# Performance work log

Measured on AMD Instinct MI355X. Metric: run time of the kernel, lower is better.

Reference implementation:

```python
import jax, jax.numpy as jnp
import numpy as np

IN_DIM = 1024
OUT_DIM = 1024
L = 4
HIDDEN = 64
EMB_DIM = 2 + 2 * 2 * L  # 18
BATCH = 8192
W0 = 30.0


def make_embedded_coords():
    gy, gx = jnp.meshgrid(jnp.linspace(-1.0, 1.0, OUT_DIM), jnp.linspace(-1.0, 1.0, IN_DIM), indexing='ij')
    coords = jnp.stack([gy, gx], axis=-1).reshape(-1, 2)  # [rows*cols, 2]
    embeds = [coords]
    for i in range(L):
        freq = 2.0 ** i
        embeds.append(jnp.sin(freq * jnp.pi * coords))
        embeds.append(jnp.cos(freq * jnp.pi * coords))
    return jnp.concatenate(embeds, axis=-1)  # [rows*cols, 18]


def setup_inputs() -> dict:
    key = jax.random.key(0)
    ks = jax.random.split(key, 8)
    # init scales matching torch code
    u = lambda k, shape, b: jax.random.uniform(k, shape, jnp.float32, -b, b)
    W1 = u(ks[0], (HIDDEN, EMB_DIM), 1.0 / EMB_DIM)
    b1 = u(ks[1], (HIDDEN,), 1.0 / np.sqrt(EMB_DIM))
    s2 = np.sqrt(6.0 / HIDDEN) / W0
    W2 = u(ks[2], (HIDDEN, HIDDEN), s2)
    b2 = u(ks[3], (HIDDEN,), 1.0 / np.sqrt(HIDDEN))
    W3 = u(ks[4], (1, HIDDEN), s2)
    b3 = u(ks[5], (1,), 1.0 / np.sqrt(HIDDEN))
    x = jax.random.normal(ks[6], (BATCH, IN_DIM), jnp.float32)
    bias = jnp.zeros((OUT_DIM,), jnp.float32)
    return {
        'x': x,
        'embedded_coords': make_embedded_coords(),
        'W1': W1, 'b1': b1, 'W2': W2, 'b2': b2, 'W3': W3, 'b3': b3,
        'bias': bias,
    }


def reference(x, embedded_coords, W1, b1, W2, b2, W3, b3, bias):
    rows = bias.shape[0]
    cols = x.shape[-1]
    # tiny fully-fused hypernet MLP over rows*cols coordinate points
    h = jnp.sin(W0 * (embedded_coords @ W1.T + b1))  # [rows*cols, 64]
    h = jnp.sin(W0 * (h @ W2.T + b2))                # [rows*cols, 64]
    W = (h @ W3.T + b3).reshape(rows, cols)          # generated weight
    return x @ W.T + bias                            # [batch, out_dim]
```

## Files before the change

kernel.cpp:

```cpp
#include <hip/hip_runtime.h>
#include <hip/hip_bf16.h>


typedef __attribute__((ext_vector_type(8))) short bf16x8;
typedef __attribute__((ext_vector_type(4))) float f32x4;

#define SIN_SCALE 4.77464829275686f

__device__ __forceinline__ unsigned short f2bf(float f) {
    union { float f; unsigned u; } v; v.f = f;
    unsigned r = v.u + 0x7fffu + ((v.u >> 16) & 1u);
    return (unsigned short)(r >> 16);
}

__device__ __forceinline__ unsigned pktrunc(float a, float b) {
    union { float f; unsigned u; } x, y; x.f = a; y.f = b;
    return (x.u >> 16) | (y.u & 0xffff0000u);
}

__device__ __forceinline__ float sinrev(float x) {
    return __builtin_amdgcn_sinf(x);
}
__device__ __forceinline__ float cosrev(float x) {
    return __builtin_amdgcn_cosf(x);
}

__device__ __forceinline__ void async_ld16(const void* g, void* l) {
    __builtin_amdgcn_global_load_lds(
        (__attribute__((address_space(1))) void*)g,
        (__attribute__((address_space(3))) void*)l, 16, 0, 0);
}

__global__ __launch_bounds__(256) void tables_kernel(
        const float* __restrict__ ec,
        const float* __restrict__ W1, const float* __restrict__ b1,
        const float* __restrict__ W2, const float* __restrict__ b2,
        float2* __restrict__ SCrow, float2* __restrict__ SCcol,
        unsigned short* __restrict__ W2bf, float* __restrict__ b2s) {
    if (blockIdx.x == 512) {
        int tid = threadIdx.x;
        #pragma unroll
        for (int q = 0; q < 16; ++q) {
            int i = q * 256 + tid;
            unsigned u = __float_as_uint(SIN_SCALE * W2[i]);
            W2bf[i] = (unsigned short)(u >> 16);
        }
        if (tid < 64) b2s[tid] = SIN_SCALE * b2[tid];
        return;
    }
    int idx = blockIdx.x * 256 + threadIdx.x;
    int j = idx & 63;
    int t = idx >> 6;
    const float* wr = W1 + j * 18;
    if (t < 1024) {
        const float* pe = ec + (long)t * 1024 * 18;
        float z = b1[j];
        #pragma unroll
        for (int i = 0; i < 18; ++i) z += wr[i] * pe[i];
        z *= SIN_SCALE;
        SCrow[t * 64 + j] = make_float2(sinrev(z), cosrev(z));
    } else {
        int c = t - 1024;
        const float* pe = ec + (long)c * 18;
        float z = 0.f;
        #pragma unroll
        for (int i = 0; i < 18; ++i) z += wr[i] * (pe[i] - ec[i]);
        z *= SIN_SCALE;
        SCcol[c * 64 + j] = make_float2(sinrev(z), cosrev(z));
    }
}

__global__ __launch_bounds__(256) void fused_cast_siren(
        const float4* __restrict__ x, unsigned short* __restrict__ xb,
        const float2* __restrict__ SCrow, const float2* __restrict__ SCcol,
        const unsigned short* __restrict__ W2bf, const float* __restrict__ b2s,
        const float* __restrict__ W3, const float* __restrict__ b3,
        unsigned short* __restrict__ Wout) {
    __shared__ __align__(16) float2 zrow_l[16 * 64];
    __shared__ __align__(16) float2 zcol_l[32 * 64];

    int tid  = threadIdx.x;
    int sb   = blockIdx.x;
    int lane = tid & 63;
    int wv   = tid >> 6;
    int ln   = lane & 15;
    int kq   = lane >> 4;

    int br = sb & 63;
    int bc = sb >> 6;

    long ci = (long)sb * 1024 + tid;

    float4 cv0 = x[ci];
    float4 cv1 = x[ci + 256];

    {
        const float* rs = (const float*)SCrow + (long)br * 16 * 128;
        #pragma unroll
        for (int q = 0; q < 2; ++q) {
            int idx = q * 256 + tid;
            async_ld16(rs + idx * 4, (float*)zrow_l + (q * 256 + wv * 64) * 4);
        }
        #pragma unroll
        for (int q = 0; q < 4; ++q) {
            int P  = q * 256 + tid;
            int cr = P >> 5;
            int pc = P & 31;
            int lc = (pc & 16) | ((pc & 15) ^ (cr & 15));
            const float* src = (const float*)SCcol + (long)(bc * 32 + cr) * 128 + lc * 4;
            async_ld16(src, (float*)zcol_l + (q * 256 + wv * 64) * 4);
        }
    }

    {
        ushort4 o;
        o.x = f2bf(cv0.x); o.y = f2bf(cv0.y); o.z = f2bf(cv0.z); o.w = f2bf(cv0.w);
        *(ushort4*)(xb + ci * 4) = o;
        o.x = f2bf(cv1.x); o.y = f2bf(cv1.y); o.z = f2bf(cv1.z); o.w = f2bf(cv1.w);
        *(ushort4*)(xb + (ci + 256) * 4) = o;
    }
    float4 cv2 = x[ci + 512];
    float4 cv3 = x[ci + 768];

    bf16x8 wfrag[2][4];
    #pragma unroll
    for (int kc = 0; kc < 2; ++kc)
        #pragma unroll
        for (int nt = 0; nt < 4; ++nt)
            wfrag[kc][nt] = *(const bf16x8*)(W2bf + (nt * 16 + ln) * 64 + kc * 32 + kq * 8);
    f32x4 b2x4[4], w3x4[4];
    #pragma unroll
    for (int nt = 0; nt < 4; ++nt) {
        float4 bb = *(const float4*)(b2s + nt * 16 + kq * 4);
        float4 ww = *(const float4*)(W3 + nt * 16 + kq * 4);
        b2x4[nt][0] = bb.x; b2x4[nt][1] = bb.y; b2x4[nt][2] = bb.z; b2x4[nt][3] = bb.w;
        w3x4[nt][0] = ww.x; w3x4[nt][1] = ww.y; w3x4[nt][2] = ww.z; w3x4[nt][3] = ww.w;
    }
    float b3s = b3[0];

    {
        ushort4 o;
        o.x = f2bf(cv2.x); o.y = f2bf(cv2.y); o.z = f2bf(cv2.z); o.w = f2bf(cv2.w);
        *(ushort4*)(xb + (ci + 512) * 4) = o;
        o.x = f2bf(cv3.x); o.y = f2bf(cv3.y); o.z = f2bf(cv3.z); o.w = f2bf(cv3.w);
        *(ushort4*)(xb + (ci + 768) * 4) = o;
    }

    __syncthreads();

    #pragma unroll
    for (int lr4 = 0; lr4 < 4; ++lr4) {
        int lr = wv * 4 + lr4;
        const float2* zb = zrow_l + lr * 64 + kq * 8;
        float sr0[8], cr0[8], sr1[8], cr1[8];
        #pragma unroll
        for (int j = 0; j < 8; ++j) {
            float2 t0 = zb[j];      sr0[j] = t0.x; cr0[j] = t0.y;
            float2 t1 = zb[32 + j]; sr1[j] = t1.x; cr1[j] = t1.y;
        }

        #pragma unroll
        for (int ct = 0; ct < 2; ++ct) {
            int cl = ct * 16 + ln;
            const float2* cb2 = zcol_l + cl * 64;
            int sx = cl & 15;

            union { bf16x8 v; unsigned u[4]; } a0, a1;
            #pragma unroll
            for (int t = 0; t < 4; ++t) {
                int p0 = (((kq * 4 + t) ^ sx)) * 2;
                int p1 = ((16 | ((kq * 4 + t) ^ sx))) * 2;
                float h0[2], h1v[2];
                #pragma unroll
                for (int e = 0; e < 2; ++e) {
                    int j = t * 2 + e;
                    float2 c0 = cb2[p0 + e];
                    float2 c1 = cb2[p1 + e];
                    h0[e]  = fmaf(sr0[j], c0.y, cr0[j] * c0.x);
                    h1v[e] = fmaf(sr1[j], c1.y, cr1[j] * c1.x);
                }
                a0.u[t] = pktrunc(h0[0], h0[1]);
                a1.u[t] = pktrunc(h1v[0], h1v[1]);
            }

            f32x4 acc[4];
            #pragma unroll
            for (int nt = 0; nt < 4; ++nt) acc[nt] = b2x4[nt];
            #pragma unroll
            for (int nt = 0; nt < 4; ++nt) {
                acc[nt] = __builtin_amdgcn_mfma_f32_16x16x32_bf16(wfrag[0][nt], a0.v, acc[nt], 0, 0, 0);
                acc[nt] = __builtin_amdgcn_mfma_f32_16x16x32_bf16(wfrag[1][nt], a1.v, acc[nt], 0, 0, 0);
            }

            float ps[4] = {0.f, 0.f, 0.f, 0.f};
            #pragma unroll
            for (int nt = 0; nt < 4; ++nt)
                #pragma unroll
                for (int rg = 0; rg < 4; ++rg)
                    ps[rg] = fmaf(w3x4[nt][rg], sinrev(acc[nt][rg]), ps[rg]);
            float s = (ps[0] + ps[1]) + (ps[2] + ps[3]);
            s += __shfl_xor(s, 32, 64);
            s += __shfl_xor(s, 16, 64);

            if (kq == 0) {
                long o = (long)(br * 16 + lr) * 1024 + bc * 32 + ct * 16 + ln;
                Wout[o] = f2bf(s + b3s);
            }
        }
    }
}

__global__ __launch_bounds__(256) void gemm_kernel(
        const unsigned short* __restrict__ A,
        const unsigned short* __restrict__ B,
        const float* __restrict__ bias,
        float* __restrict__ C) {
    const int K = 1024;
    __shared__ __align__(16) unsigned short As[2][128 * 64];
    __shared__ __align__(16) unsigned short Bs[2][128 * 64];

    int tid  = threadIdx.x;
    int lane = tid & 63;
    int wv   = tid >> 6;
    int wm   = wv & 1, wn = wv >> 1;
    long Abase = (long)blockIdx.x * 128 * K;
    long Bbase = (long)blockIdx.y * 128 * K;

    int sr8 = tid >> 3;
    int sl  = tid & 7;
    int rsel = lane & 15;
    int kq   = lane >> 4;

    f32x4 acc[4][4] = {};

    auto stage = [&](int kt, int sbuf) {
        #pragma unroll
        for (int q = 0; q < 4; ++q) {
            int row = q * 32 + sr8;
            int cc  = sl ^ (row & 7);
            const unsigned short* ga = A + Abase + (long)row * K + kt + cc * 8;
            const unsigned short* gb = B + Bbase + (long)row * K + kt + cc * 8;
            unsigned short* la = &As[sbuf][(q * 256 + wv * 64) * 8];
            unsigned short* lb = &Bs[sbuf][(q * 256 + wv * 64) * 8];
            async_ld16(ga, la);
            async_ld16(gb, lb);
        }
    };

    auto compute = [&](int sbuf) {
        #pragma unroll
        for (int h = 0; h < 2; ++h) {
            bf16x8 af[4], bf[4];
            #pragma unroll
            for (int mi = 0; mi < 4; ++mi) {
                int row = wm * 64 + mi * 16 + rsel;
                int ch  = (h * 4 + kq) ^ (row & 7);
                af[mi] = *(const bf16x8*)&As[sbuf][row * 64 + ch * 8];
            }
            #pragma unroll
            for (int ni = 0; ni < 4; ++ni) {
                int row = wn * 64 + ni * 16 + rsel;
                int ch  = (h * 4 + kq) ^ (row & 7);
                bf[ni] = *(const bf16x8*)&Bs[sbuf][row * 64 + ch * 8];
            }
            #pragma unroll
            for (int mi = 0; mi < 4; ++mi)
                #pragma unroll
                for (int ni = 0; ni < 4; ++ni)
                    acc[mi][ni] = __builtin_amdgcn_mfma_f32_16x16x32_bf16(
                        af[mi], bf[ni], acc[mi][ni], 0, 0, 0);
        }
    };

    stage(0, 0);
    __syncthreads();
    int buf = 0;
    for (int kt = 64; kt < K; kt += 64) {
        stage(kt, buf ^ 1);
        compute(buf);
        __syncthreads();
        buf ^= 1;
    }
    compute(buf);

    int row0 = blockIdx.x * 128 + wm * 64;
    int col0 = blockIdx.y * 128 + wn * 64;
    #pragma unroll
    for (int ni = 0; ni < 4; ++ni) {
        int col = col0 + ni * 16 + rsel;
        float bv = bias[col];
        #pragma unroll
        for (int mi = 0; mi < 4; ++mi) {
            int rbase = row0 + mi * 16 + kq * 4;
            #pragma unroll
            for (int r = 0; r < 4; ++r)
                C[(long)(rbase + r) * 1024 + col] = acc[mi][ni][r] + bv;
        }
    }
}

extern "C" void kernel_launch(void* const* d_in, const int* in_sizes, int n_in,
                              void* d_out, int out_size, void* d_ws, size_t ws_size,
                              hipStream_t stream) {
    const float* x    = (const float*)d_in[0];
    const float* ec   = (const float*)d_in[1];
    const float* W1   = (const float*)d_in[2];
    const float* b1   = (const float*)d_in[3];
    const float* W2   = (const float*)d_in[4];
    const float* b2   = (const float*)d_in[5];
    const float* W3   = (const float*)d_in[6];
    const float* b3   = (const float*)d_in[7];
    const float* bias = (const float*)d_in[8];
    float* out = (float*)d_out;

    unsigned short* xb = (unsigned short*)d_ws;
    unsigned short* Wb = xb + (size_t)8192 * 1024;
    float2* SCrow = (float2*)(Wb + (size_t)1024 * 1024);
    float2* SCcol = SCrow + 1024 * 64;
    unsigned short* W2bf = (unsigned short*)(SCcol + 1024 * 64);
    float* b2s = (float*)(W2bf + 4096);

    tables_kernel<<<513, 256, 0, stream>>>(ec, W1, b1, W2, b2, SCrow, SCcol, W2bf, b2s);
    fused_cast_siren<<<2048, 256, 0, stream>>>((const float4*)x, xb, SCrow, SCcol,
                                               W2bf, b2s, W3, b3, Wb);
    dim3 g(64, 8);
    gemm_kernel<<<g, 256, 0, stream>>>(xb, Wb, bias, out);
}
```

Baseline: 183.6 us.

## Process four tiles per block with double-buffered LDS and pipelined loads

Each block of the fused cast/SIREN kernel now handles four consecutive tiles instead of one, and the grid shrinks from 2048 to 512 blocks. LDS tables are double-buffered, so the async loads of the next tile's row/column sin-cos tables and the next chunk of x overlap with the MFMA compute of the current tile. The bf16 cast stores for x are interleaved into the same software pipeline. This spreads the per-block setup (W2 fragments, biases) over more work. It doubles LDS per block and cuts the number of resident waves, which may reduce latency hiding for the memory-bound x cast.

```diff
diff --git a/kernel.cpp b/kernel.cpp
--- a/kernel.cpp
+++ b/kernel.cpp
@@ -76,30 +76,25 @@
         const unsigned short* __restrict__ W2bf, const float* __restrict__ b2s,
         const float* __restrict__ W3, const float* __restrict__ b3,
         unsigned short* __restrict__ Wout) {
-    __shared__ __align__(16) float2 zrow_l[16 * 64];
-    __shared__ __align__(16) float2 zcol_l[32 * 64];
+    __shared__ __align__(16) float2 zrow_l[2][16 * 64];
+    __shared__ __align__(16) float2 zcol_l[2][32 * 64];
 
     int tid  = threadIdx.x;
-    int sb   = blockIdx.x;
     int lane = tid & 63;
     int wv   = tid >> 6;
     int ln   = lane & 15;
     int kq   = lane >> 4;
 
-    int br = sb & 63;
-    int bc = sb >> 6;
-
-    long ci = (long)sb * 1024 + tid;
-
-    float4 cv0 = x[ci];
-    float4 cv1 = x[ci + 256];
-
-    {
+    int sb0 = blockIdx.x * 4;
+    long ci0 = (long)sb0 * 1024 + tid;
+
+    auto stage = [&](int st, int b) {
+        int br = st & 63, bc = st >> 6;
         const float* rs = (const float*)SCrow + (long)br * 16 * 128;
         #pragma unroll
         for (int q = 0; q < 2; ++q) {
             int idx = q * 256 + tid;
-            async_ld16(rs + idx * 4, (float*)zrow_l + (q * 256 + wv * 64) * 4);
+            async_ld16(rs + idx * 4, (float*)&zrow_l[b][0] + (q * 256 + wv * 64) * 4);
         }
         #pragma unroll
         for (int q = 0; q < 4; ++q) {
@@ -108,19 +103,29 @@
             int pc = P & 31;
             int lc = (pc & 16) | ((pc & 15) ^ (cr & 15));
             const float* src = (const float*)SCcol + (long)(bc * 32 + cr) * 128 + lc * 4;
-            async_ld16(src, (float*)zcol_l + (q * 256 + wv * 64) * 4);
-        }
-    }
-
-    {
+            async_ld16(src, (float*)&zcol_l[b][0] + (q * 256 + wv * 64) * 4);
+        }
+    };
+
+    auto cld = [&](long ci, float4& v0, float4& v1, float4& v2, float4& v3) {
+        v0 = x[ci]; v1 = x[ci + 256]; v2 = x[ci + 512]; v3 = x[ci + 768];
+    };
+    auto cst = [&](long ci, const float4& v0, const float4& v1,
+                   const float4& v2, const float4& v3) {
         ushort4 o;
-        o.x = f2bf(cv0.x); o.y = f2bf(cv0.y); o.z = f2bf(cv0.z); o.w = f2bf(cv0.w);
+        o.x = f2bf(v0.x); o.y = f2bf(v0.y); o.z = f2bf(v0.z); o.w = f2bf(v0.w);
         *(ushort4*)(xb + ci * 4) = o;
-        o.x = f2bf(cv1.x); o.y = f2bf(cv1.y); o.z = f2bf(cv1.z); o.w = f2bf(cv1.w);
+        o.x = f2bf(v1.x); o.y = f2bf(v1.y); o.z = f2bf(v1.z); o.w = f2bf(v1.w);
         *(ushort4*)(xb + (ci + 256) * 4) = o;
-    }
-    float4 cv2 = x[ci + 512];
-    float4 cv3 = x[ci + 768];
+        o.x = f2bf(v2.x); o.y = f2bf(v2.y); o.z = f2bf(v2.z); o.w = f2bf(v2.w);
+        *(ushort4*)(xb + (ci + 512) * 4) = o;
+        o.x = f2bf(v3.x); o.y = f2bf(v3.y); o.z = f2bf(v3.z); o.w = f2bf(v3.w);
+        *(ushort4*)(xb + (ci + 768) * 4) = o;
+    };
+
+    float4 cA0, cA1, cA2, cA3, cB0, cB1, cB2, cB3;
+    cld(ci0, cA0, cA1, cA2, cA3);
+    stage(sb0, 0);
 
     bf16x8 wfrag[2][4];
     #pragma unroll
@@ -138,76 +143,92 @@
     }
     float b3s = b3[0];
 
-    {
-        ushort4 o;
-        o.x = f2bf(cv2.x); o.y = f2bf(cv2.y); o.z = f2bf(cv2.z); o.w = f2bf(cv2.w);
-        *(ushort4*)(xb + (ci + 512) * 4) = o;
-        o.x = f2bf(cv3.x); o.y = f2bf(cv3.y); o.z = f2bf(cv3.z); o.w = f2bf(cv3.w);
-        *(ushort4*)(xb + (ci + 768) * 4) = o;
-    }
-
-    __syncthreads();
-
-    #pragma unroll
-    for (int lr4 = 0; lr4 < 4; ++lr4) {
-        int lr = wv * 4 + lr4;
-        const float2* zb = zrow_l + lr * 64 + kq * 8;
-        float sr0[8], cr0[8], sr1[8], cr1[8];
-        #pragma unroll
-        for (int j = 0; j < 8; ++j) {
-            float2 t0 = zb[j];      sr0[j] = t0.x; cr0[j] = t0.y;
-            float2 t1 = zb[32 + j]; sr1[j] = t1.x; cr1[j] = t1.y;
-        }
-
-        #pragma unroll
-        for (int ct = 0; ct < 2; ++ct) {
-            int cl = ct * 16 + ln;
-            const float2* cb2 = zcol_l + cl * 64;
-            int sx = cl & 15;
-
-            union { bf16x8 v; unsigned u[4]; } a0, a1;
-            #pragma unroll
-            for (int t = 0; t < 4; ++t) {
-                int p0 = (((kq * 4 + t) ^ sx)) * 2;
-                int p1 = ((16 | ((kq * 4 + t) ^ sx))) * 2;
-                float h0[2], h1v[2];
-                #pragma unroll
-                for (int e = 0; e < 2; ++e) {
-                    int j = t * 2 + e;
-                    float2 c0 = cb2[p0 + e];
-                    float2 c1 = cb2[p1 + e];
-                    h0[e]  = fmaf(sr0[j], c0.y, cr0[j] * c0.x);
-                    h1v[e] = fmaf(sr1[j], c1.y, cr1[j] * c1.x);
+    auto compute = [&](int st, int b) {
+        int br = st & 63, bc = st >> 6;
+        #pragma unroll
+        for (int lr4 = 0; lr4 < 4; ++lr4) {
+            int lr = wv * 4 + lr4;
+            const float2* zb = &zrow_l[b][lr * 64 + kq * 8];
+            float sr0[8], cr0[8], sr1[8], cr1[8];
+            #pragma unroll
+            for (int j = 0; j < 8; ++j) {
+                float2 t0 = zb[j];      sr0[j] = t0.x; cr0[j] = t0.y;
+                float2 t1 = zb[32 + j]; sr1[j] = t1.x; cr1[j] = t1.y;
+            }
+
+            #pragma unroll
+            for (int ct = 0; ct < 2; ++ct) {
+                int cl = ct * 16 + ln;
+                const float2* cb2 = &zcol_l[b][cl * 64];
+                int sx = cl & 15;
+
+                union { bf16x8 v; unsigned u[4]; } a0, a1;
+                #pragma unroll
+                for (int t = 0; t < 4; ++t) {
+                    int p0 = (((kq * 4 + t) ^ sx)) * 2;
+                    int p1 = ((16 | ((kq * 4 + t) ^ sx))) * 2;
+                    float h0[2], h1v[2];
+                    #pragma unroll
+                    for (int e = 0; e < 2; ++e) {
+                        int j = t * 2 + e;
+                        float2 c0 = cb2[p0 + e];
+                        float2 c1 = cb2[p1 + e];
+                        h0[e]  = fmaf(sr0[j], c0.y, cr0[j] * c0.x);
+                        h1v[e] = fmaf(sr1[j], c1.y, cr1[j] * c1.x);
+                    }
+                    a0.u[t] = pktrunc(h0[0], h0[1]);
+                    a1.u[t] = pktrunc(h1v[0], h1v[1]);
                 }
-                a0.u[t] = pktrunc(h0[0], h0[1]);
-                a1.u[t] = pktrunc(h1v[0], h1v[1]);
+
+                f32x4 acc[4];
+                #pragma unroll
+                for (int nt = 0; nt < 4; ++nt) acc[nt] = b2x4[nt];
+                #pragma unroll
+                for (int nt = 0; nt < 4; ++nt) {
+                    acc[nt] = __builtin_amdgcn_mfma_f32_16x16x32_bf16(wfrag[0][nt], a0.v, acc[nt], 0, 0, 0);
+                    acc[nt] = __builtin_amdgcn_mfma_f32_16x16x32_bf16(wfrag[1][nt], a1.v, acc[nt], 0, 0, 0);
+                }
+
+                float ps[4] = {0.f, 0.f, 0.f, 0.f};
+                #pragma unroll
+                for (int nt = 0; nt < 4; ++nt)
+                    #pragma unroll
+                    for (int rg = 0; rg < 4; ++rg)
+                        ps[rg] = fmaf(w3x4[nt][rg], sinrev(acc[nt][rg]), ps[rg]);
+                float s = (ps[0] + ps[1]) + (ps[2] + ps[3]);
+                s += __shfl_xor(s, 32, 64);
+                s += __shfl_xor(s, 16, 64);
+
+                if (kq == 0) {
+                    long o = (long)(br * 16 + lr) * 1024 + bc * 32 + ct * 16 + ln;
+                    Wout[o] = f2bf(s + b3s);
+                }
             }
-
-            f32x4 acc[4];
-            #pragma unroll
-            for (int nt = 0; nt < 4; ++nt) acc[nt] = b2x4[nt];
-            #pragma unroll
-            for (int nt = 0; nt < 4; ++nt) {
-                acc[nt] = __builtin_amdgcn_mfma_f32_16x16x32_bf16(wfrag[0][nt], a0.v, acc[nt], 0, 0, 0);
-                acc[nt] = __builtin_amdgcn_mfma_f32_16x16x32_bf16(wfrag[1][nt], a1.v, acc[nt], 0, 0, 0);
-            }
-
-            float ps[4] = {0.f, 0.f, 0.f, 0.f};
-            #pragma unroll
-            for (int nt = 0; nt < 4; ++nt)
-                #pragma unroll
-                for (int rg = 0; rg < 4; ++rg)
-                    ps[rg] = fmaf(w3x4[nt][rg], sinrev(acc[nt][rg]), ps[rg]);
-            float s = (ps[0] + ps[1]) + (ps[2] + ps[3]);
-            s += __shfl_xor(s, 32, 64);
-            s += __shfl_xor(s, 16, 64);
-
-            if (kq == 0) {
-                long o = (long)(br * 16 + lr) * 1024 + bc * 32 + ct * 16 + ln;
-                Wout[o] = f2bf(s + b3s);
-            }
-        }
-    }
+        }
+    };
+
+    __syncthreads();
+
+    cst(ci0, cA0, cA1, cA2, cA3);
+    cld(ci0 + 1024, cB0, cB1, cB2, cB3);
+    stage(sb0 + 1, 1);
+    compute(sb0 + 0, 0);
+    __syncthreads();
+
+    cst(ci0 + 1024, cB0, cB1, cB2, cB3);
+    cld(ci0 + 2048, cA0, cA1, cA2, cA3);
+    stage(sb0 + 2, 0);
+    compute(sb0 + 1, 1);
+    __syncthreads();
+
+    cst(ci0 + 2048, cA0, cA1, cA2, cA3);
+    cld(ci0 + 3072, cB0, cB1, cB2, cB3);
+    stage(sb0 + 3, 1);
+    compute(sb0 + 2, 0);
+    __syncthreads();
+
+    cst(ci0 + 3072, cB0, cB1, cB2, cB3);
+    compute(sb0 + 3, 1);
 }
 
 __global__ __launch_bounds__(256) void gemm_kernel(
@@ -321,8 +342,8 @@
     float* b2s = (float*)(W2bf + 4096);
 
     tables_kernel<<<513, 256, 0, stream>>>(ec, W1, b1, W2, b2, SCrow, SCcol, W2bf, b2s);
-    fused_cast_siren<<<2048, 256, 0, stream>>>((const float4*)x, xb, SCrow, SCcol,
-                                               W2bf, b2s, W3, b3, Wb);
+    fused_cast_siren<<<512, 256, 0, stream>>>((const float4*)x, xb, SCrow, SCcol,
+                                              W2bf, b2s, W3, b3, Wb);
     dim3 g(64, 8);
     gemm_kernel<<<g, 256, 0, stream>>>(xb, Wb, bias, out);
 }
```

New measurement: 188.4 us. 1.03x slower.

## Fuse fp32-to-bf16 cast of x into GEMM A-tile loading

Applied to the files above, without the earlier changes.

Drops the separate bf16 copy of x that the SIREN kernel wrote. The GEMM now loads fp32 x into registers, converts it to bf16, and writes it into swizzled LDS, with the global loads for the next tile issued before compute. This avoids writing and re-reading the 16 MB bf16 copy of x. In exchange the GEMM reads fp32 A (twice the bytes of bf16, re-read by each of the 8 column blocks) and uses more registers, with a synchronous register path in place of async LDS loads for A.

```diff
diff --git a/kernel.cpp b/kernel.cpp
--- a/kernel.cpp
+++ b/kernel.cpp
@@ -70,8 +70,7 @@
     }
 }
 
-__global__ __launch_bounds__(256) void fused_cast_siren(
-        const float4* __restrict__ x, unsigned short* __restrict__ xb,
+__global__ __launch_bounds__(256) void siren_w_kernel(
         const float2* __restrict__ SCrow, const float2* __restrict__ SCcol,
         const unsigned short* __restrict__ W2bf, const float* __restrict__ b2s,
         const float* __restrict__ W3, const float* __restrict__ b3,
@@ -88,11 +87,6 @@
 
     int br = sb & 63;
     int bc = sb >> 6;
-
-    long ci = (long)sb * 1024 + tid;
-
-    float4 cv0 = x[ci];
-    float4 cv1 = x[ci + 256];
 
     {
         const float* rs = (const float*)SCrow + (long)br * 16 * 128;
@@ -111,16 +105,6 @@
             async_ld16(src, (float*)zcol_l + (q * 256 + wv * 64) * 4);
         }
     }
-
-    {
-        ushort4 o;
-        o.x = f2bf(cv0.x); o.y = f2bf(cv0.y); o.z = f2bf(cv0.z); o.w = f2bf(cv0.w);
-        *(ushort4*)(xb + ci * 4) = o;
-        o.x = f2bf(cv1.x); o.y = f2bf(cv1.y); o.z = f2bf(cv1.z); o.w = f2bf(cv1.w);
-        *(ushort4*)(xb + (ci + 256) * 4) = o;
-    }
-    float4 cv2 = x[ci + 512];
-    float4 cv3 = x[ci + 768];
 
     bf16x8 wfrag[2][4];
     #pragma unroll
@@ -137,14 +121,6 @@
         w3x4[nt][0] = ww.x; w3x4[nt][1] = ww.y; w3x4[nt][2] = ww.z; w3x4[nt][3] = ww.w;
     }
     float b3s = b3[0];
-
-    {
-        ushort4 o;
-        o.x = f2bf(cv2.x); o.y = f2bf(cv2.y); o.z = f2bf(cv2.z); o.w = f2bf(cv2.w);
-        *(ushort4*)(xb + (ci + 512) * 4) = o;
-        o.x = f2bf(cv3.x); o.y = f2bf(cv3.y); o.z = f2bf(cv3.z); o.w = f2bf(cv3.w);
-        *(ushort4*)(xb + (ci + 768) * 4) = o;
-    }
 
     __syncthreads();
 
@@ -211,7 +187,7 @@
 }
 
 __global__ __launch_bounds__(256) void gemm_kernel(
-        const unsigned short* __restrict__ A,
+        const float* __restrict__ X,
         const unsigned short* __restrict__ B,
         const float* __restrict__ bias,
         float* __restrict__ C) {
@@ -223,7 +199,7 @@
     int lane = tid & 63;
     int wv   = tid >> 6;
     int wm   = wv & 1, wn = wv >> 1;
-    long Abase = (long)blockIdx.x * 128 * K;
+    long Xbase = (long)blockIdx.x * 128 * K;
     long Bbase = (long)blockIdx.y * 128 * K;
 
     int sr8 = tid >> 3;
@@ -231,19 +207,39 @@
     int rsel = lane & 15;
     int kq   = lane >> 4;
 
+    int arow = tid >> 1;
+    int acol = (tid & 1) * 32;
+
     f32x4 acc[4][4] = {};
 
-    auto stage = [&](int kt, int sbuf) {
+    auto stageB = [&](int kt, int sbuf) {
         #pragma unroll
         for (int q = 0; q < 4; ++q) {
             int row = q * 32 + sr8;
             int cc  = sl ^ (row & 7);
-            const unsigned short* ga = A + Abase + (long)row * K + kt + cc * 8;
             const unsigned short* gb = B + Bbase + (long)row * K + kt + cc * 8;
-            unsigned short* la = &As[sbuf][(q * 256 + wv * 64) * 8];
             unsigned short* lb = &Bs[sbuf][(q * 256 + wv * 64) * 8];
-            async_ld16(ga, la);
             async_ld16(gb, lb);
+        }
+    };
+
+    auto ldA = [&](int kt, float4* va) {
+        const float* src = X + Xbase + (long)arow * K + kt + acol;
+        #pragma unroll
+        for (int q = 0; q < 8; ++q) va[q] = *(const float4*)(src + q * 4);
+    };
+    auto wrA = [&](int sbuf, const float4* va) {
+        #pragma unroll
+        for (int q2 = 0; q2 < 4; ++q2) {
+            int lc = (acol >> 3) + q2;
+            union { bf16x8 v; unsigned u[4]; } t;
+            #pragma unroll
+            for (int h = 0; h < 2; ++h) {
+                float4 v = va[q2 * 2 + h];
+                t.u[h * 2 + 0] = (unsigned)f2bf(v.x) | ((unsigned)f2bf(v.y) << 16);
+                t.u[h * 2 + 1] = (unsigned)f2bf(v.z) | ((unsigned)f2bf(v.w) << 16);
+            }
+            *(bf16x8*)&As[sbuf][arow * 64 + (lc ^ (arow & 7)) * 8] = t.v;
         }
     };
 
@@ -272,12 +268,17 @@
         }
     };
 
-    stage(0, 0);
+    float4 va[8];
+    ldA(0, va);
+    stageB(0, 0);
+    wrA(0, va);
     __syncthreads();
     int buf = 0;
     for (int kt = 64; kt < K; kt += 64) {
-        stage(kt, buf ^ 1);
+        ldA(kt, va);
+        stageB(kt, buf ^ 1);
         compute(buf);
+        wrA(buf ^ 1, va);
         __syncthreads();
         buf ^= 1;
     }
@@ -313,16 +314,14 @@
     const float* bias = (const float*)d_in[8];
     float* out = (float*)d_out;
 
-    unsigned short* xb = (unsigned short*)d_ws;
-    unsigned short* Wb = xb + (size_t)8192 * 1024;
+    unsigned short* Wb = (unsigned short*)d_ws;
     float2* SCrow = (float2*)(Wb + (size_t)1024 * 1024);
     float2* SCcol = SCrow + 1024 * 64;
     unsigned short* W2bf = (unsigned short*)(SCcol + 1024 * 64);
     float* b2s = (float*)(W2bf + 4096);
 
     tables_kernel<<<513, 256, 0, stream>>>(ec, W1, b1, W2, b2, SCrow, SCcol, W2bf, b2s);
-    fused_cast_siren<<<2048, 256, 0, stream>>>((const float4*)x, xb, SCrow, SCcol,
-                                               W2bf, b2s, W3, b3, Wb);
+    siren_w_kernel<<<2048, 256, 0, stream>>>(SCrow, SCcol, W2bf, b2s, W3, b3, Wb);
     dim3 g(64, 8);
-    gemm_kernel<<<g, 256, 0, stream>>>(xb, Wb, bias, out);
-}
+    gemm_kernel<<<g, 256, 0, stream>>>(x, Wb, bias, out);
+}
```

After: 212.3 us. +15.6%, slower.
